# Optimization experiments

Hardware: AMD Instinct MI355X
Metric: run time of the kernel (lower is better)

Reference implementation:

```python
import jax, jax.numpy as jnp
import numpy as np
from jax import lax

L, H, NUM_CONVS, KSIZE = 8192, 128, 4, 7
EPS = 1e-5


def _pos_encoding(length, dim, dtype):
    pos = jnp.arange(length, dtype=jnp.float32)[:, None]
    i = jnp.arange(dim, dtype=jnp.float32)[None, :]
    angle = pos / jnp.power(10000.0, (2.0 * jnp.floor(i / 2.0)) / dim)
    pe = jnp.where((jnp.arange(dim) % 2 == 0)[None, :], jnp.sin(angle), jnp.cos(angle))
    return pe.astype(dtype)


def _layer_norm(x):
    mu = jnp.mean(x, axis=-1, keepdims=True)
    var = jnp.mean(jnp.square(x - mu), axis=-1, keepdims=True)
    return (x - mu) * lax.rsqrt(var + EPS)


def _conv1d_same(x, w, b):
    # x: [L, H]; w: [H_out, H_in, K]; b: [H_out]. SAME padding over sequence.
    lhs = x.T[None]  # [1, H, L]
    out = lax.conv_general_dilated(lhs, w, window_strides=(1,), padding='SAME',
                                   dimension_numbers=('NCH', 'OIH', 'NCH'))
    return (out[0] + b[:, None]).T  # [L, H]


def setup_inputs() -> dict:
    key = jax.random.key(0)
    ks = jax.random.split(key, 12)
    s = 0.02
    return {
        'x': jax.random.normal(ks[0], (L, H), jnp.float32),
        'conv_w': jax.random.normal(ks[1], (NUM_CONVS, H, H, KSIZE), jnp.float32) * s,
        'conv_b': jax.random.normal(ks[2], (NUM_CONVS, H), jnp.float32) * s,
        'Wq': jax.random.normal(ks[3], (H, H), jnp.float32) * s,
        'bq': jax.random.normal(ks[4], (H,), jnp.float32) * s,
        'Wk': jax.random.normal(ks[5], (H, H), jnp.float32) * s,
        'bk': jax.random.normal(ks[6], (H,), jnp.float32) * s,
        'Wv': jax.random.normal(ks[7], (H, H), jnp.float32) * s,
        'bv': jax.random.normal(ks[8], (H,), jnp.float32) * s,
        'Wff': jax.random.normal(ks[9], (H, H), jnp.float32) * s,
        'bff': jax.random.normal(ks[10], (H,), jnp.float32) * s,
    }


def reference(x, conv_w, conv_b, Wq, bq, Wk, bk, Wv, bv, Wff, bff):
    h = x + _pos_encoding(x.shape[0], x.shape[1], x.dtype)
    # conv stack: LN -> conv -> residual, repeated num_convs times
    for i in range(NUM_CONVS):
        residual = h
        h = _conv1d_same(_layer_norm(h), conv_w[i], conv_b[i]) + residual
    # self-attention (single-head as written in the source)
    residual = h
    n = _layer_norm(h)
    q = n @ Wq.T + bq
    k = n @ Wk.T + bk
    v = n @ Wv.T + bv
    scale = 1.0 / jnp.sqrt(jnp.asarray(H, h.dtype))
    attn = jax.nn.softmax((q @ k.T) * scale, axis=-1)  # [L, L]
    h = attn @ v + residual
    # feed-forward
    residual = h
    h = jax.nn.relu(_layer_norm(h) @ Wff.T + bff) + residual
    return h
```

## Files before the change

### kernel.cpp

```cpp
#include <hip/hip_runtime.h>

#define LL 8192
#define HH 128

typedef __attribute__((ext_vector_type(8))) short short8v;
typedef __attribute__((ext_vector_type(4))) short short4v;
typedef __attribute__((ext_vector_type(4))) float f32x4;
typedef __attribute__((ext_vector_type(16))) float f32x16;

__device__ inline short f2bf(float f) {
    union { float f; unsigned u; } x; x.f = f;
    unsigned r = (x.u + 0x7fffu + ((x.u >> 16) & 1u)) >> 16;
    return (short)r;
}
__device__ inline float bf2f(short s) {
    union { unsigned u; float f; } x; x.u = ((unsigned)(unsigned short)s) << 16;
    return x.f;
}

__device__ inline void plane32swap(unsigned& a, unsigned& b) {
#if defined(__has_builtin)
#if __has_builtin(__builtin_amdgcn_permlane32_swap)
    typedef unsigned u2v __attribute__((ext_vector_type(2)));
    u2v r = __builtin_amdgcn_permlane32_swap(a, b, false, false);
    a = r[0]; b = r[1];
    return;
#endif
#endif
    asm volatile("v_permlane32_swap_b32 %0, %1" : "+v"(a), "+v"(b));
}

__device__ inline short* sAp(short* base, int row, int col) {
    int byte = (row << 8) + (col << 1);
    byte ^= (row & 7) << 4;
    return (short*)((char*)base + byte);
}

__device__ inline short8v ln_pack8(const float* rowF, int l15) {
    const float4 a = *(const float4*)&rowF[l15 * 8];
    const float4 b = *(const float4*)&rowF[l15 * 8 + 4];
    float s  = (a.x + a.y) + (a.z + a.w) + (b.x + b.y) + (b.z + b.w);
    float s2 = a.x * a.x + a.y * a.y + a.z * a.z + a.w * a.w
             + b.x * b.x + b.y * b.y + b.z * b.z + b.w * b.w;
#pragma unroll
    for (int off = 1; off <= 8; off <<= 1) {
        s  += __shfl_xor(s,  off, 64);
        s2 += __shfl_xor(s2, off, 64);
    }
    float mu = s * (1.f / 128.f);
    float var = s2 * (1.f / 128.f) - mu * mu;
    float rstd = rsqrtf(var + 1e-5f);
    short8v r;
    r[0] = f2bf((a.x - mu) * rstd);
    r[1] = f2bf((a.y - mu) * rstd);
    r[2] = f2bf((a.z - mu) * rstd);
    r[3] = f2bf((a.w - mu) * rstd);
    r[4] = f2bf((b.x - mu) * rstd);
    r[5] = f2bf((b.y - mu) * rstd);
    r[6] = f2bf((b.z - mu) * rstd);
    r[7] = f2bf((b.w - mu) * rstd);
    return r;
}

__global__ __launch_bounds__(256) void repack_all(const float* __restrict__ x,
                                                  const float* __restrict__ w,
                                                  const float* __restrict__ Wq,
                                                  const float* __restrict__ Wk,
                                                  const float* __restrict__ Wv,
                                                  const float* __restrict__ bq,
                                                  const float* __restrict__ bk,
                                                  const float* __restrict__ bv,
                                                  const float* __restrict__ Wff,
                                                  short* __restrict__ wkb,
                                                  short* __restrict__ wqkvb,
                                                  float* __restrict__ b3,
                                                  short* __restrict__ wffb,
                                                  float* __restrict__ h0) {
    const float qs = 0.08838834764831845f;
    int idx = blockIdx.x * 256 + threadIdx.x;
    if (idx < 458752) {
        int k = idx % 7;
        int t = idx / 7;
        int i = t % HH; t /= HH;
        int o = t % HH;
        int lay = t / HH;
        wkb[((lay * 7 + k) * HH + o) * HH + i] = f2bf(w[idx]);
    } else {
        int j = idx - 458752;
        if (j < 49152) {
            int t = j >> 14, r = j & 16383;
            float v = (t == 0) ? Wq[r] * qs : (t == 1) ? Wk[r] : Wv[r];
            wqkvb[j] = f2bf(v);
        } else if (j < 49536) {
            int jj = j - 49152;
            b3[jj] = (jj < 128) ? bq[jj] * qs : (jj < 256) ? bk[jj - 128] : bv[jj - 256];
        } else if (j < 65920) {
            int jj = j - 49536;
            wffb[jj] = f2bf(Wff[jj]);
        } else {
            int p = j - 65920;
            if (p < 262144) {
                int g = p >> 5, c4 = (p & 31) << 2;
                float4 val = *(const float4*)&x[g * HH + c4];
                float fg = (float)g;
#pragma unroll
                for (int h = 0; h < 2; h++) {
                    int i0 = c4 + h * 2;
                    float e = (float)i0 / 128.f;
                    float ang = fg / powf(10000.f, e);
                    ((float*)&val)[h * 2]     += sinf(ang);
                    ((float*)&val)[h * 2 + 1] += cosf(ang);
                }
                *(float4*)&h0[g * HH + c4] = val;
            }
        }
    }
}

__global__ __launch_bounds__(256, 4) void conv_layer_kernel(const float* __restrict__ hin,
                                                            const short* __restrict__ wkb,
                                                            const float* __restrict__ conv_b,
                                                            float* __restrict__ hout,
                                                            int lay) {
    __shared__ float sF[22][132];
    __shared__ short sA[22 * 128];
    int tid = threadIdx.x;
    int w = tid >> 6, lane = tid & 63;
    int l15 = lane & 15, quad = lane >> 4;
    int m0 = (blockIdx.x >> 1) * 16;
    int c0w = (blockIdx.x & 1) * 64 + w * 16;

    for (int idx = tid; idx < 22 * 32; idx += 256) {
        int r = idx >> 5, c4 = (idx & 31) << 2;
        int g = m0 - 3 + r;
        float4 val = make_float4(0.f, 0.f, 0.f, 0.f);
        if (g >= 0 && g < LL) val = *(const float4*)&hin[g * HH + c4];
        *(float4*)&sF[r][c4] = val;
    }
    __syncthreads();
#pragma unroll
    for (int rr = 0; rr < 2; rr++) {
        int row = rr * 16 + w * 4 + quad;
        if (row < 22)
            *(short8v*)sAp(sA, row, l15 * 8) = ln_pack8(&sF[row][0], l15);
    }
    __syncthreads();
    f32x4 accA = (f32x4)(0.f), accB = (f32x4)(0.f);
    const short* wl = wkb + lay * 7 * HH * HH;
    for (int k = 0; k < 7; k++) {
        const short* b0 = wl + (k * HH + c0w + l15) * HH;
#pragma unroll
        for (int ks = 0; ks < 4; ks++) {
            short8v bf = *(const short8v*)&b0[ks * 32 + quad * 8];
            short8v af = *(const short8v*)sAp(sA, l15 + k, ks * 32 + quad * 8);
            if (ks & 1) accB = __builtin_amdgcn_mfma_f32_16x16x32_bf16(af, bf, accB, 0, 0, 0);
            else        accA = __builtin_amdgcn_mfma_f32_16x16x32_bf16(af, bf, accA, 0, 0, 0);
        }
    }
    float bb = conv_b[lay * HH + c0w + l15];
#pragma unroll
    for (int r = 0; r < 4; r++) {
        int row = quad * 4 + r;
        hout[(m0 + row) * HH + c0w + l15] =
            sF[3 + row][c0w + l15] + accA[r] + accB[r] + bb;
    }
}

__global__ __launch_bounds__(256, 4) void qkv_kernel(const float* __restrict__ h4,
                                                     const short* __restrict__ wqkvb,
                                                     const float* __restrict__ b3,
                                                     short* __restrict__ qb,
                                                     short* __restrict__ kb,
                                                     short* __restrict__ vt) {
    __shared__ float sF[16][132];
    __shared__ short sA[16 * 128];
    __shared__ short sT[4][32][17];
    int tid = threadIdx.x;
    int w = tid >> 6, lane = tid & 63;
    int l15 = lane & 15, quad = lane >> 4;
    int m0 = blockIdx.x * 16;
    int t = blockIdx.y;

    for (int idx = tid; idx < 16 * 32; idx += 256) {
        int r = idx >> 5, c4 = (idx & 31) << 2;
        *(float4*)&sF[r][c4] = *(const float4*)&h4[(m0 + r) * HH + c4];
    }
    __syncthreads();
    {
        int row = w * 4 + quad;
        *(short8v*)sAp(sA, row, l15 * 8) = ln_pack8(&sF[row][0], l15);
    }
    __syncthreads();
    int c0 = w * 32;
    f32x4 acc0 = (f32x4)(0.f), acc1 = (f32x4)(0.f);
    const short* b0 = wqkvb + (t * 128 + c0 + l15) * HH;
    const short* b1 = b0 + 16 * HH;
#pragma unroll
    for (int ks = 0; ks < 4; ks++) {
        short8v af = *(const short8v*)sAp(sA, l15, ks * 32 + quad * 8);
        short8v bf0 = *(const short8v*)&b0[ks * 32 + quad * 8];
        short8v bf1 = *(const short8v*)&b1[ks * 32 + quad * 8];
        acc0 = __builtin_amdgcn_mfma_f32_16x16x32_bf16(af, bf0, acc0, 0, 0, 0);
        acc1 = __builtin_amdgcn_mfma_f32_16x16x32_bf16(af, bf1, acc1, 0, 0, 0);
    }
    float bb0 = b3[t * 128 + c0 + l15], bb1 = b3[t * 128 + c0 + 16 + l15];
    if (t < 2) {
        short* o = (t == 0) ? qb : kb;
#pragma unroll
        for (int r = 0; r < 4; r++) {
            int lr = m0 + quad * 4 + r;
            o[lr * HH + c0 + l15]      = f2bf(acc0[r] + bb0);
            o[lr * HH + c0 + 16 + l15] = f2bf(acc1[r] + bb1);
        }
    } else {
#pragma unroll
        for (int r = 0; r < 4; r++) {
            sT[w][l15][quad * 4 + r]      = f2bf(acc0[r] + bb0);
            sT[w][16 + l15][quad * 4 + r] = f2bf(acc1[r] + bb1);
        }
        asm volatile("s_waitcnt lgkmcnt(0)" ::: "memory");
#pragma unroll
        for (int cc = 0; cc < 8; cc++) {
            int col = cc * 4 + quad;
            vt[(c0 + col) * LL + m0 + l15] = sT[w][col][l15];
        }
    }
}

#define FBN 64

__global__ __launch_bounds__(256, 2) void flash_mfma_kernel(const short* __restrict__ qs,
                                                            const short* __restrict__ ksrc,
                                                            const short* __restrict__ vsrc,
                                                            short* __restrict__ PO,
                                                            float* __restrict__ Pl,
                                                            int segrows) {
    __shared__ short sK[16 * 64 * 8];
    __shared__ short sV[16 * 64 * 8];

    const int tid = threadIdx.x;
    const int w = tid >> 6, lane = tid & 63;
    const int l31 = lane & 31, hi = lane >> 5;
    const int m0 = blockIdx.x * 128;
    const int seg = blockIdx.y;
    const int jbeg = seg * segrows;
    const int nchunk = segrows >> 6;
    const int qrow = m0 + w * 32 + l31;

    short8v qf[8];
#pragma unroll
    for (int ks = 0; ks < 8; ks++)
        qf[ks] = *(const short8v*)&qs[qrow * HH + ks * 16 + hi * 8];

    float l_r = 0.f;
    f32x16 o_acc[4];
#pragma unroll
    for (int dt = 0; dt < 4; dt++) o_acc[dt] = (f32x16)(0.f);

    short8v kr[4], vr[4];
#pragma unroll
    for (int r = 0; r < 4; r++) {
        int s = w + 4 * r;
        kr[r] = *(const short8v*)&ksrc[(jbeg + (s >> 3) * 32 + l31) * HH + (s & 7) * 16 + hi * 8];
        vr[r] = *(const short8v*)&vsrc[((s >> 2) * 32 + l31) * LL + jbeg + (s & 3) * 16 + hi * 8];
    }

    for (int c = 0; c < nchunk; c++) {
        __syncthreads();
#pragma unroll
        for (int r = 0; r < 4; r++) {
            int s = w + 4 * r;
            *(short8v*)&sK[(s * 64 + lane) * 8] = kr[r];
            *(short8v*)&sV[(s * 64 + lane) * 8] = vr[r];
        }
        __syncthreads();
        if (c + 1 < nchunk) {
            const int j1 = jbeg + (c + 1) * FBN;
#pragma unroll
            for (int r = 0; r < 4; r++) {
                int s = w + 4 * r;
                kr[r] = *(const short8v*)&ksrc[(j1 + (s >> 3) * 32 + l31) * HH + (s & 7) * 16 + hi * 8];
                vr[r] = *(const short8v*)&vsrc[((s >> 2) * 32 + l31) * LL + j1 + (s & 3) * 16 + hi * 8];
            }
        }
        f32x16 s0 = (f32x16)(0.f), s1 = (f32x16)(0.f);
#pragma unroll
        for (int ks = 0; ks < 8; ks++) {
            short8v kf0 = *(const short8v*)&sK[((ks) * 64 + lane) * 8];
            short8v kf1 = *(const short8v*)&sK[((8 + ks) * 64 + lane) * 8];
            s0 = __builtin_amdgcn_mfma_f32_32x32x16_bf16(kf0, qf[ks], s0, 0, 0, 0);
            s1 = __builtin_amdgcn_mfma_f32_32x32x16_bf16(kf1, qf[ks], s1, 0, 0, 0);
        }
        short8v pfrag[4];
#pragma unroll
        for (int nt = 0; nt < 2; nt++) {
            const f32x16& sa = nt ? s1 : s0;
            unsigned pw[8];
#pragma unroll
            for (int m = 0; m < 8; m++) {
                float p0 = __expf(fminf(sa[2 * m], 30.f));
                float p1 = __expf(fminf(sa[2 * m + 1], 30.f));
                l_r += p0 + p1;
                union { float f; unsigned u; } u0, u1;
                u0.f = p0; u1.f = p1;
                pw[m] = (u0.u >> 16) | (u1.u & 0xffff0000u);
            }
            plane32swap(pw[0], pw[2]);
            plane32swap(pw[1], pw[3]);
            plane32swap(pw[4], pw[6]);
            plane32swap(pw[5], pw[7]);
            union { unsigned u[4]; short8v v; } fa, fb;
            fa.u[0] = pw[0]; fa.u[1] = pw[1]; fa.u[2] = pw[2]; fa.u[3] = pw[3];
            fb.u[0] = pw[4]; fb.u[1] = pw[5]; fb.u[2] = pw[6]; fb.u[3] = pw[7];
            pfrag[nt * 2]     = fa.v;
            pfrag[nt * 2 + 1] = fb.v;
        }
#pragma unroll
        for (int ks = 0; ks < 4; ks++)
#pragma unroll
            for (int dt = 0; dt < 4; dt++) {
                short8v vf = *(const short8v*)&sV[((dt * 4 + ks) * 64 + lane) * 8];
                o_acc[dt] = __builtin_amdgcn_mfma_f32_32x32x16_bf16(pfrag[ks], vf, o_acc[dt], 0, 0, 0);
            }
    }
    float lsum = l_r + __shfl_xor(l_r, 32, 64);
    if (hi == 0)
        Pl[seg * LL + qrow] = lsum;
#pragma unroll
    for (int dt = 0; dt < 4; dt++)
#pragma unroll
        for (int i = 0; i < 16; i++) {
            int qr = (i & 3) + 8 * (i >> 2) + 4 * hi;
            PO[(size_t)seg * LL * HH + (size_t)(m0 + w * 32 + qr) * HH + dt * 32 + l31] =
                f2bf(o_acc[dt][i]);
        }
}

__global__ __launch_bounds__(256) void ff_kernel(const float* __restrict__ hin,
                                                 const short* __restrict__ PO,
                                                 const float* __restrict__ Pl,
                                                 const short* __restrict__ wffb,
                                                 const float* __restrict__ bff,
                                                 float* __restrict__ out,
                                                 int nsplit) {
    __shared__ float sF[16][132];
    __shared__ short sA[16 * 128];
    __shared__ float sLi[16];
    int tid = threadIdx.x;
    int w = tid >> 6, lane = tid & 63;
    int l15 = lane & 15, quad = lane >> 4;
    int m0 = blockIdx.x * 16;

    if (tid < 16) {
        float s = 0.f;
        for (int seg = 0; seg < nsplit; seg++) s += Pl[seg * LL + m0 + tid];
        sLi[tid] = 1.f / s;
    }
    __syncthreads();
    for (int idx = tid; idx < 16 * 32; idx += 256) {
        int r = idx >> 5, c4 = (idx & 31) << 2;
        float4 hv = *(const float4*)&hin[(m0 + r) * HH + c4];
        float s0 = 0.f, s1 = 0.f, s2 = 0.f, s3 = 0.f;
        for (int seg = 0; seg < nsplit; seg++) {
            short4v pv = *(const short4v*)&PO[(size_t)seg * LL * HH + (m0 + r) * HH + c4];
            s0 += bf2f(pv[0]); s1 += bf2f(pv[1]); s2 += bf2f(pv[2]); s3 += bf2f(pv[3]);
        }
        float li = sLi[r];
        *(float4*)&sF[r][c4] = make_float4(hv.x + s0 * li, hv.y + s1 * li,
                                           hv.z + s2 * li, hv.w + s3 * li);
    }
    __syncthreads();
    {
        int row = w * 4 + quad;
        *(short8v*)sAp(sA, row, l15 * 8) = ln_pack8(&sF[row][0], l15);
    }
    __syncthreads();
    int c0 = w * 32;
    f32x4 acc0 = (f32x4)(0.f), acc1 = (f32x4)(0.f);
    const short* b0 = wffb + (c0 + l15) * HH;
    const short* b1 = b0 + 16 * HH;
#pragma unroll
    for (int ks = 0; ks < 4; ks++) {
        short8v af = *(const short8v*)sAp(sA, l15, ks * 32 + quad * 8);
        short8v bf0 = *(const short8v*)&b0[ks * 32 + quad * 8];
        short8v bf1 = *(const short8v*)&b1[ks * 32 + quad * 8];
        acc0 = __builtin_amdgcn_mfma_f32_16x16x32_bf16(af, bf0, acc0, 0, 0, 0);
        acc1 = __builtin_amdgcn_mfma_f32_16x16x32_bf16(af, bf1, acc1, 0, 0, 0);
    }
    float bb0 = bff[c0 + l15], bb1 = bff[c0 + 16 + l15];
#pragma unroll
    for (int r = 0; r < 4; r++) {
        int lr = quad * 4 + r;
        out[(m0 + lr) * HH + c0 + l15]      = fmaxf(acc0[r] + bb0, 0.f) + sF[lr][c0 + l15];
        out[(m0 + lr) * HH + c0 + 16 + l15] = fmaxf(acc1[r] + bb1, 0.f) + sF[lr][c0 + 16 + l15];
    }
}

extern "C" void kernel_launch(void* const* d_in, const int* in_sizes, int n_in,
                              void* d_out, int out_size, void* d_ws, size_t ws_size,
                              hipStream_t stream) {
    const float* x      = (const float*)d_in[0];
    const float* conv_w = (const float*)d_in[1];
    const float* conv_b = (const float*)d_in[2];
    const float* Wq = (const float*)d_in[3];
    const float* bq = (const float*)d_in[4];
    const float* Wk = (const float*)d_in[5];
    const float* bk = (const float*)d_in[6];
    const float* Wv = (const float*)d_in[7];
    const float* bv = (const float*)d_in[8];
    const float* Wff = (const float*)d_in[9];
    const float* bff = (const float*)d_in[10];
    float* out = (float*)d_out;

    char* ws = (char*)d_ws;
    const size_t MB = 1u << 20;
    float* hB   = (float*)(ws);
    short* qb   = (short*)(ws + 4 * MB);
    short* kb   = (short*)(ws + 6 * MB);
    short* vt   = (short*)(ws + 8 * MB);
    float* Pl   = (float*)(ws + 10 * MB);
    short* wffb = (short*)(ws + 10 * MB + 524288);
    short* PO   = (short*)(ws + 10 * MB + 524288 + 32768);
    short* wkb   = (short*)(ws + 16 * MB);
    short* wqkvb = (short*)(ws + 17 * MB);
    float* b3    = (float*)(ws + 17 * MB + 131072);
    float* h0    = (float*)(ws + 18 * MB);
    float* h13   = (float*)(ws + 22 * MB);
    float* h2    = h0;

    const int nsplit = 8;
    const int segrows = LL / nsplit;

    repack_all<<<3074, 256, 0, stream>>>(x, conv_w, Wq, Wk, Wv, bq, bk, bv, Wff,
                                         wkb, wqkvb, b3, wffb, h0);
    conv_layer_kernel<<<LL / 16 * 2, 256, 0, stream>>>(h0,  wkb, conv_b, h13, 0);
    conv_layer_kernel<<<LL / 16 * 2, 256, 0, stream>>>(h13, wkb, conv_b, h2,  1);
    conv_layer_kernel<<<LL / 16 * 2, 256, 0, stream>>>(h2,  wkb, conv_b, h13, 2);
    conv_layer_kernel<<<LL / 16 * 2, 256, 0, stream>>>(h13, wkb, conv_b, hB,  3);
    qkv_kernel<<<dim3(LL / 16, 3), 256, 0, stream>>>(hB, wqkvb, b3, qb, kb, vt);
    flash_mfma_kernel<<<dim3(LL / 128, nsplit), 256, 0, stream>>>(qb, kb, vt, PO, Pl, segrows);
    ff_kernel<<<LL / 16, 256, 0, stream>>>(hB, PO, Pl, wffb, bff, out, nsplit);
}
```

Measured before the change: 214.7 us.

## Fuse last conv layer with QKV projection; double-buffer K/V tiles in flash kernel

The fourth conv layer and the QKV projection now run in one kernel. Each block computes 16 output rows across all 128 channels, re-normalises them from shared memory and produces Q, K and V without re-reading hB or relaunching. This removes one launch and the hB round trip, but the conv layer now runs on half as many blocks, with each wave covering 32 columns instead of 16. The flash attention kernel also double-buffers its K/V LDS tiles, so one barrier per chunk replaces two, at the cost of twice the shared memory.

```diff
diff --git a/kernel.cpp b/kernel.cpp
--- a/kernel.cpp
+++ b/kernel.cpp
@@ -166,63 +166,107 @@
     }
 }
 
-__global__ __launch_bounds__(256, 4) void qkv_kernel(const float* __restrict__ h4,
-                                                     const short* __restrict__ wqkvb,
-                                                     const float* __restrict__ b3,
-                                                     short* __restrict__ qb,
-                                                     short* __restrict__ kb,
-                                                     short* __restrict__ vt) {
-    __shared__ float sF[16][132];
-    __shared__ short sA[16 * 128];
+__global__ __launch_bounds__(256, 2) void conv_qkv_kernel(const float* __restrict__ hin,
+                                                          const short* __restrict__ wkb,
+                                                          const float* __restrict__ conv_b,
+                                                          const short* __restrict__ wqkvb,
+                                                          const float* __restrict__ b3,
+                                                          float* __restrict__ hB,
+                                                          short* __restrict__ qb,
+                                                          short* __restrict__ kb,
+                                                          short* __restrict__ vt) {
+    __shared__ float sF[22][132];
+    __shared__ short sA[22 * 128];
     __shared__ short sT[4][32][17];
     int tid = threadIdx.x;
     int w = tid >> 6, lane = tid & 63;
     int l15 = lane & 15, quad = lane >> 4;
     int m0 = blockIdx.x * 16;
-    int t = blockIdx.y;
-
-    for (int idx = tid; idx < 16 * 32; idx += 256) {
+    int c0 = w * 32;
+
+    for (int idx = tid; idx < 22 * 32; idx += 256) {
         int r = idx >> 5, c4 = (idx & 31) << 2;
-        *(float4*)&sF[r][c4] = *(const float4*)&h4[(m0 + r) * HH + c4];
+        int g = m0 - 3 + r;
+        float4 val = make_float4(0.f, 0.f, 0.f, 0.f);
+        if (g >= 0 && g < LL) val = *(const float4*)&hin[g * HH + c4];
+        *(float4*)&sF[r][c4] = val;
+    }
+    __syncthreads();
+#pragma unroll
+    for (int rr = 0; rr < 2; rr++) {
+        int row = rr * 16 + w * 4 + quad;
+        if (row < 22)
+            *(short8v*)sAp(sA, row, l15 * 8) = ln_pack8(&sF[row][0], l15);
+    }
+    __syncthreads();
+    f32x4 a0 = (f32x4)(0.f), a1 = (f32x4)(0.f);
+    const short* wl = wkb + 3 * 7 * HH * HH;
+    for (int k = 0; k < 7; k++) {
+        const short* b0 = wl + (k * HH + c0 + l15) * HH;
+        const short* b1 = b0 + 16 * HH;
+#pragma unroll
+        for (int ks = 0; ks < 4; ks++) {
+            short8v bf0 = *(const short8v*)&b0[ks * 32 + quad * 8];
+            short8v bf1 = *(const short8v*)&b1[ks * 32 + quad * 8];
+            short8v af = *(const short8v*)sAp(sA, l15 + k, ks * 32 + quad * 8);
+            a0 = __builtin_amdgcn_mfma_f32_16x16x32_bf16(af, bf0, a0, 0, 0, 0);
+            a1 = __builtin_amdgcn_mfma_f32_16x16x32_bf16(af, bf1, a1, 0, 0, 0);
+        }
+    }
+    float bb0 = conv_b[3 * HH + c0 + l15], bb1 = conv_b[3 * HH + c0 + 16 + l15];
+#pragma unroll
+    for (int r = 0; r < 4; r++) {
+        int row = quad * 4 + r;
+        float v0 = sF[3 + row][c0 + l15]      + a0[r] + bb0;
+        float v1 = sF[3 + row][c0 + 16 + l15] + a1[r] + bb1;
+        sF[3 + row][c0 + l15]      = v0;
+        sF[3 + row][c0 + 16 + l15] = v1;
+        hB[(m0 + row) * HH + c0 + l15]      = v0;
+        hB[(m0 + row) * HH + c0 + 16 + l15] = v1;
     }
     __syncthreads();
     {
         int row = w * 4 + quad;
-        *(short8v*)sAp(sA, row, l15 * 8) = ln_pack8(&sF[row][0], l15);
-    }
-    __syncthreads();
-    int c0 = w * 32;
-    f32x4 acc0 = (f32x4)(0.f), acc1 = (f32x4)(0.f);
-    const short* b0 = wqkvb + (t * 128 + c0 + l15) * HH;
-    const short* b1 = b0 + 16 * HH;
-#pragma unroll
-    for (int ks = 0; ks < 4; ks++) {
-        short8v af = *(const short8v*)sAp(sA, l15, ks * 32 + quad * 8);
-        short8v bf0 = *(const short8v*)&b0[ks * 32 + quad * 8];
-        short8v bf1 = *(const short8v*)&b1[ks * 32 + quad * 8];
-        acc0 = __builtin_amdgcn_mfma_f32_16x16x32_bf16(af, bf0, acc0, 0, 0, 0);
-        acc1 = __builtin_amdgcn_mfma_f32_16x16x32_bf16(af, bf1, acc1, 0, 0, 0);
-    }
-    float bb0 = b3[t * 128 + c0 + l15], bb1 = b3[t * 128 + c0 + 16 + l15];
-    if (t < 2) {
-        short* o = (t == 0) ? qb : kb;
-#pragma unroll
-        for (int r = 0; r < 4; r++) {
-            int lr = m0 + quad * 4 + r;
-            o[lr * HH + c0 + l15]      = f2bf(acc0[r] + bb0);
-            o[lr * HH + c0 + 16 + l15] = f2bf(acc1[r] + bb1);
-        }
-    } else {
-#pragma unroll
-        for (int r = 0; r < 4; r++) {
-            sT[w][l15][quad * 4 + r]      = f2bf(acc0[r] + bb0);
-            sT[w][16 + l15][quad * 4 + r] = f2bf(acc1[r] + bb1);
-        }
-        asm volatile("s_waitcnt lgkmcnt(0)" ::: "memory");
-#pragma unroll
-        for (int cc = 0; cc < 8; cc++) {
-            int col = cc * 4 + quad;
-            vt[(c0 + col) * LL + m0 + l15] = sT[w][col][l15];
+        *(short8v*)sAp(sA, row, l15 * 8) = ln_pack8(&sF[3 + row][0], l15);
+    }
+    __syncthreads();
+    short8v af4[4];
+#pragma unroll
+    for (int ks = 0; ks < 4; ks++)
+        af4[ks] = *(const short8v*)sAp(sA, l15, ks * 32 + quad * 8);
+
+    for (int t = 0; t < 3; t++) {
+        f32x4 acc0 = (f32x4)(0.f), acc1 = (f32x4)(0.f);
+        const short* b0 = wqkvb + (t * 128 + c0 + l15) * HH;
+        const short* b1 = b0 + 16 * HH;
+#pragma unroll
+        for (int ks = 0; ks < 4; ks++) {
+            short8v bf0 = *(const short8v*)&b0[ks * 32 + quad * 8];
+            short8v bf1 = *(const short8v*)&b1[ks * 32 + quad * 8];
+            acc0 = __builtin_amdgcn_mfma_f32_16x16x32_bf16(af4[ks], bf0, acc0, 0, 0, 0);
+            acc1 = __builtin_amdgcn_mfma_f32_16x16x32_bf16(af4[ks], bf1, acc1, 0, 0, 0);
+        }
+        float qb0 = b3[t * 128 + c0 + l15], qb1 = b3[t * 128 + c0 + 16 + l15];
+        if (t < 2) {
+            short* o = (t == 0) ? qb : kb;
+#pragma unroll
+            for (int r = 0; r < 4; r++) {
+                int lr = m0 + quad * 4 + r;
+                o[lr * HH + c0 + l15]      = f2bf(acc0[r] + qb0);
+                o[lr * HH + c0 + 16 + l15] = f2bf(acc1[r] + qb1);
+            }
+        } else {
+#pragma unroll
+            for (int r = 0; r < 4; r++) {
+                sT[w][l15][quad * 4 + r]      = f2bf(acc0[r] + qb0);
+                sT[w][16 + l15][quad * 4 + r] = f2bf(acc1[r] + qb1);
+            }
+            asm volatile("s_waitcnt lgkmcnt(0)" ::: "memory");
+#pragma unroll
+            for (int cc = 0; cc < 8; cc++) {
+                int col = cc * 4 + quad;
+                vt[(c0 + col) * LL + m0 + l15] = sT[w][col][l15];
+            }
         }
     }
 }
@@ -235,8 +279,8 @@
                                                             short* __restrict__ PO,
                                                             float* __restrict__ Pl,
                                                             int segrows) {
-    __shared__ short sK[16 * 64 * 8];
-    __shared__ short sV[16 * 64 * 8];
+    __shared__ short sK[2 * 16 * 64 * 8];
+    __shared__ short sV[2 * 16 * 64 * 8];
 
     const int tid = threadIdx.x;
     const int w = tid >> 6, lane = tid & 63;
@@ -264,32 +308,51 @@
         kr[r] = *(const short8v*)&ksrc[(jbeg + (s >> 3) * 32 + l31) * HH + (s & 7) * 16 + hi * 8];
         vr[r] = *(const short8v*)&vsrc[((s >> 2) * 32 + l31) * LL + jbeg + (s & 3) * 16 + hi * 8];
     }
-
-    for (int c = 0; c < nchunk; c++) {
-        __syncthreads();
+#pragma unroll
+    for (int r = 0; r < 4; r++) {
+        int s = w + 4 * r;
+        *(short8v*)&sK[(s * 64 + lane) * 8] = kr[r];
+        *(short8v*)&sV[(s * 64 + lane) * 8] = vr[r];
+    }
+    if (nchunk > 1) {
+        const int j1 = jbeg + FBN;
 #pragma unroll
         for (int r = 0; r < 4; r++) {
             int s = w + 4 * r;
-            *(short8v*)&sK[(s * 64 + lane) * 8] = kr[r];
-            *(short8v*)&sV[(s * 64 + lane) * 8] = vr[r];
-        }
-        __syncthreads();
+            kr[r] = *(const short8v*)&ksrc[(j1 + (s >> 3) * 32 + l31) * HH + (s & 7) * 16 + hi * 8];
+            vr[r] = *(const short8v*)&vsrc[((s >> 2) * 32 + l31) * LL + j1 + (s & 3) * 16 + hi * 8];
+        }
+    }
+    __syncthreads();
+
+    int cur = 0;
+    for (int c = 0; c < nchunk; c++) {
+        const int kb_ = cur * 8192;
+        f32x16 s0 = (f32x16)(0.f), s1 = (f32x16)(0.f);
+#pragma unroll
+        for (int ks = 0; ks < 8; ks++) {
+            short8v kf0 = *(const short8v*)&sK[kb_ + ((ks) * 64 + lane) * 8];
+            short8v kf1 = *(const short8v*)&sK[kb_ + ((8 + ks) * 64 + lane) * 8];
+            s0 = __builtin_amdgcn_mfma_f32_32x32x16_bf16(kf0, qf[ks], s0, 0, 0, 0);
+            s1 = __builtin_amdgcn_mfma_f32_32x32x16_bf16(kf1, qf[ks], s1, 0, 0, 0);
+        }
         if (c + 1 < nchunk) {
-            const int j1 = jbeg + (c + 1) * FBN;
+            const int nb = (cur ^ 1) * 8192;
 #pragma unroll
             for (int r = 0; r < 4; r++) {
                 int s = w + 4 * r;
-                kr[r] = *(const short8v*)&ksrc[(j1 + (s >> 3) * 32 + l31) * HH + (s & 7) * 16 + hi * 8];
-                vr[r] = *(const short8v*)&vsrc[((s >> 2) * 32 + l31) * LL + j1 + (s & 3) * 16 + hi * 8];
-            }
-        }
-        f32x16 s0 = (f32x16)(0.f), s1 = (f32x16)(0.f);
-#pragma unroll
-        for (int ks = 0; ks < 8; ks++) {
-            short8v kf0 = *(const short8v*)&sK[((ks) * 64 + lane) * 8];
-            short8v kf1 = *(const short8v*)&sK[((8 + ks) * 64 + lane) * 8];
-            s0 = __builtin_amdgcn_mfma_f32_32x32x16_bf16(kf0, qf[ks], s0, 0, 0, 0);
-            s1 = __builtin_amdgcn_mfma_f32_32x32x16_bf16(kf1, qf[ks], s1, 0, 0, 0);
+                *(short8v*)&sK[nb + (s * 64 + lane) * 8] = kr[r];
+                *(short8v*)&sV[nb + (s * 64 + lane) * 8] = vr[r];
+            }
+            if (c + 2 < nchunk) {
+                const int j2 = jbeg + (c + 2) * FBN;
+#pragma unroll
+                for (int r = 0; r < 4; r++) {
+                    int s = w + 4 * r;
+                    kr[r] = *(const short8v*)&ksrc[(j2 + (s >> 3) * 32 + l31) * HH + (s & 7) * 16 + hi * 8];
+                    vr[r] = *(const short8v*)&vsrc[((s >> 2) * 32 + l31) * LL + j2 + (s & 3) * 16 + hi * 8];
+                }
+            }
         }
         short8v pfrag[4];
 #pragma unroll
@@ -319,9 +382,11 @@
         for (int ks = 0; ks < 4; ks++)
 #pragma unroll
             for (int dt = 0; dt < 4; dt++) {
-                short8v vf = *(const short8v*)&sV[((dt * 4 + ks) * 64 + lane) * 8];
+                short8v vf = *(const short8v*)&sV[kb_ + ((dt * 4 + ks) * 64 + lane) * 8];
                 o_acc[dt] = __builtin_amdgcn_mfma_f32_32x32x16_bf16(pfrag[ks], vf, o_acc[dt], 0, 0, 0);
             }
+        __syncthreads();
+        cur ^= 1;
     }
     float lsum = l_r + __shfl_xor(l_r, 32, 64);
     if (hi == 0)
@@ -436,8 +501,8 @@
     conv_layer_kernel<<<LL / 16 * 2, 256, 0, stream>>>(h0,  wkb, conv_b, h13, 0);
     conv_layer_kernel<<<LL / 16 * 2, 256, 0, stream>>>(h13, wkb, conv_b, h2,  1);
     conv_layer_kernel<<<LL / 16 * 2, 256, 0, stream>>>(h2,  wkb, conv_b, h13, 2);
-    conv_layer_kernel<<<LL / 16 * 2, 256, 0, stream>>>(h13, wkb, conv_b, hB,  3);
-    qkv_kernel<<<dim3(LL / 16, 3), 256, 0, stream>>>(hB, wqkvb, b3, qb, kb, vt);
+    conv_qkv_kernel<<<LL / 16, 256, 0, stream>>>(h13, wkb, conv_b, wqkvb, b3,
+                                                 hB, qb, kb, vt);
     flash_mfma_kernel<<<dim3(LL / 128, nsplit), 256, 0, stream>>>(qb, kb, vt, PO, Pl, segrows);
     ff_kernel<<<LL / 16, 256, 0, stream>>>(hB, PO, Pl, wffb, bff, out, nsplit);
 }
```

Measured after the change: 211.6 us. Within noise of the previous version (-1.4%).
